# Kernel tuning notes

Hardware: AMD Instinct MI355X
Metric: run time of the kernel (lower is better)

## Reference

```python
import jax, jax.numpy as jnp
import numpy as np

NINP, NHID, K = 300, 64, 2   # input dim, hidden dim, pyramid levels (from Net.__init__)
GH = NHID // K               # per-pyramid-level width contributed to each gate (32)
S, B = 512, 256              # seq_len, batch


def setup_inputs() -> dict:
    key = jax.random.key(0)
    k = jax.random.split(key, 5)
    s = 0.05
    return {
        "x": jax.random.normal(k[0], (S, B, NINP), jnp.float32),
        "h0": jnp.zeros((B, NHID), jnp.float32),
        "c0": jnp.zeros((B, NHID), jnp.float32),
        "W_pt0": jax.random.normal(k[1], (NINP, 4 * GH), jnp.float32) * s,
        "b_pt0": jnp.zeros((4 * GH,), jnp.float32),
        "W_pt1": jax.random.normal(k[2], (NINP // 2, 4 * GH), jnp.float32) * s,
        "b_pt1": jnp.zeros((4 * GH,), jnp.float32),
        "W_glt": jax.random.normal(k[3], (1, NHID, 4 * NHID), jnp.float32) * s,  # g=1 grouped linear
        "W_dec": jax.random.normal(k[4], (NHID, 3), jnp.float32) * s,
        "b_dec": jnp.zeros((3,), jnp.float32),
    }


def _pyramidal_i2h(x, W_pt0, b_pt0, W_pt1, b_pt1):
    # Pyramidal transform: level 0 = full-res input, level 1 = features avg-pooled by 2.
    # Each level produces 4*GH gate features; levels are concatenated per gate -> NHID.
    x1 = x.reshape(x.shape[0], x.shape[1], NINP // 2, 2).mean(-1)  # (S,B,150)
    g0 = (x @ W_pt0 + b_pt0).reshape(x.shape[0], x.shape[1], 4, GH)
    g1 = (x1 @ W_pt1 + b_pt1).reshape(x.shape[0], x.shape[1], 4, GH)
    return jnp.concatenate([g0, g1], axis=-1)  # (S,B,4,NHID) gates order: f,g,i,o


def reference(x, h0, c0, W_pt0, b_pt0, W_pt1, b_pt1, W_glt, W_dec, b_dec):
    # Precompute input-to-hidden gate contributions for all timesteps (same math as per-step).
    i2h = _pyramidal_i2h(x, W_pt0, b_pt0, W_pt1, b_pt1)  # (S,B,4,NHID)
    bsz = h0.shape[0]

    def step(carry, i2h_t):
        h, c = carry
        # grouped linear (g=1): (B,1,NHID) x (1,NHID,4*NHID) -> (B,4,NHID)
        h2h = jnp.einsum('bgi,gio->bgo', h.reshape(bsz, 1, NHID), W_glt).reshape(bsz, 4, NHID)
        gates = i2h_t + h2h
        f, g, i, o = gates[:, 0], gates[:, 1], gates[:, 2], gates[:, 3]
        c1 = jax.nn.sigmoid(f) * c + jax.nn.sigmoid(i) * jnp.tanh(g)
        h1 = jax.nn.sigmoid(o) * jnp.tanh(c1)
        return (h1, c1), h1

    (hT, cT), hs = jax.lax.scan(step, (h0, c0), i2h)  # hs: (S,B,NHID)
    decoded = hs @ W_dec + b_dec                       # (S,B,3)
    return decoded, hT, cT
```

## Files before the change

### kernel.cpp

```cpp
#include <hip/hip_runtime.h>
#include <hip/hip_bf16.h>

#define SLEN 512
#define BATCH 256
#define NIN 300
#define KP 320
#define NG 256
#define NH 64
#define BM 128
#define BN 128
#define BK 64
#define LDP 72

typedef float f32x4 __attribute__((ext_vector_type(4)));
typedef _Float16 f16x8 __attribute__((ext_vector_type(8)));
typedef _Float16 f16x4 __attribute__((ext_vector_type(4)));

__global__ void prep_w(const float* __restrict__ Wpt0, const float* __restrict__ bpt0,
                       const float* __restrict__ Wpt1, const float* __restrict__ bpt1,
                       const float* __restrict__ Wglt,
                       _Float16* __restrict__ Wc16, float* __restrict__ bcat,
                       _Float16* __restrict__ Wg16) {
  int idx = blockIdx.x * 256 + threadIdx.x;
  if (idx < NG * KP) {
    int n = idx / KP, k = idx - n * KP;
    int g = n >> 6, h = n & 63;
    float w = 0.f;
    if (k < NIN) {
      if (h < 32) w = Wpt0[k * 128 + g * 32 + h];
      else        w = 0.5f * Wpt1[(k >> 1) * 128 + g * 32 + (h - 32)];
    }
    Wc16[idx] = (_Float16)w;
  }
  if (idx < NG * NH) {
    int c = idx >> 6, k = idx & 63;
    Wg16[idx] = (_Float16)Wglt[k * NG + c];
  }
  if (idx < NG) {
    int g = idx >> 6, h = idx & 63;
    bcat[idx] = (h < 32) ? bpt0[g * 32 + h] : bpt1[g * 32 + h - 32];
  }
}

__global__ __launch_bounds__(256) void gemm_i2h(
    const float* __restrict__ x, const _Float16* __restrict__ Wc16,
    const float* __restrict__ bcat, _Float16* __restrict__ C) {
  __shared__ _Float16 As[BM][LDP];
  __shared__ _Float16 Bs[BN][LDP];
  const int tid = threadIdx.x;
  const int m0 = blockIdx.y * BM;
  const int n0 = blockIdx.x * BN;
  const int lane = tid & 63;
  const int w = tid >> 6;
  const int wr = w >> 1, wc = w & 1;

  f32x4 acc[4][4];
#pragma unroll
  for (int m = 0; m < 4; ++m)
#pragma unroll
    for (int n = 0; n < 4; ++n) acc[m][n] = (f32x4){0.f, 0.f, 0.f, 0.f};

  const int arow_l = tid >> 4;
  const int acol   = (tid & 15) * 4;
  const int brow_l = tid >> 3;
  const int bcol   = (tid & 7) * 8;

  for (int k0 = 0; k0 < KP; k0 += BK) {
#pragma unroll
    for (int p = 0; p < 8; ++p) {
      int row = p * 16 + arow_l;
      int gk = k0 + acol;
      f32x4 v = (f32x4){0.f, 0.f, 0.f, 0.f};
      if (gk + 3 < NIN)
        v = *reinterpret_cast<const f32x4*>(&x[(size_t)(m0 + row) * NIN + gk]);
      f16x4 sv;
      sv[0] = (_Float16)v[0]; sv[1] = (_Float16)v[1];
      sv[2] = (_Float16)v[2]; sv[3] = (_Float16)v[3];
      *reinterpret_cast<f16x4*>(&As[row][acol]) = sv;
    }
#pragma unroll
    for (int p = 0; p < 4; ++p) {
      int n = p * 32 + brow_l;
      f16x8 v = *reinterpret_cast<const f16x8*>(&Wc16[(size_t)(n0 + n) * KP + k0 + bcol]);
      *reinterpret_cast<f16x8*>(&Bs[n][bcol]) = v;
    }
    __syncthreads();
#pragma unroll
    for (int ks = 0; ks < 2; ++ks) {
      const int kk = ks * 32 + (lane >> 4) * 8;
      f16x8 a[4], b[4];
#pragma unroll
      for (int m = 0; m < 4; ++m)
        a[m] = *reinterpret_cast<const f16x8*>(&As[wr * 64 + m * 16 + (lane & 15)][kk]);
#pragma unroll
      for (int n = 0; n < 4; ++n)
        b[n] = *reinterpret_cast<const f16x8*>(&Bs[wc * 64 + n * 16 + (lane & 15)][kk]);
#pragma unroll
      for (int m = 0; m < 4; ++m)
#pragma unroll
        for (int n = 0; n < 4; ++n)
          acc[m][n] = __builtin_amdgcn_mfma_f32_16x16x32_f16(a[m], b[n], acc[m][n], 0, 0, 0);
    }
    __syncthreads();
  }
  const int fc = lane & 15;
  const int fr = (lane >> 4) * 4;
#pragma unroll
  for (int n = 0; n < 4; ++n) {
    int col = n0 + wc * 64 + n * 16 + fc;
    float bias = bcat[col];
#pragma unroll
    for (int m = 0; m < 4; ++m) {
#pragma unroll
      for (int r = 0; r < 4; ++r) {
        int row = m0 + wr * 64 + m * 16 + fr + r;
        C[(size_t)row * NG + col] = (_Float16)(acc[m][n][r] + bias);
      }
    }
  }
}

__global__ __launch_bounds__(256, 4)
void rec_seq(
    const _Float16* __restrict__ i2h, const _Float16* __restrict__ Wg16,
    const float* __restrict__ h_in, const float* __restrict__ c_in,
    float* __restrict__ h_state, float* __restrict__ c_state,
    _Float16* __restrict__ hs_out, float* __restrict__ hT_out, float* __restrict__ cT_out,
    int T, int is_last) {
  const int b = blockIdx.x;
  const int tid = threadIdx.x;
  const int ww = tid >> 6;
  const int l = tid & 63;
  const int g = l >> 4;
  const int hidx = ww * 16 + (l & 15);
  const int col = g * 64 + hidx;

  __shared__ __align__(16) char LB[8 * NG * 16];
  f16x8* Wst = reinterpret_cast<f16x8*>(LB);
  _Float16* hbuf = reinterpret_cast<_Float16*>(LB);

  for (int e = tid; e < 8 * NG; e += 256) {
    int kk = e >> 8, c = e & 255;
    Wst[e] = *reinterpret_cast<const f16x8*>(Wg16 + (size_t)c * NH + kk * 8);
  }
  __syncthreads();

  f16x8 w0 = Wst[0 * NG + col], w1 = Wst[1 * NG + col];
  f16x8 w2 = Wst[2 * NG + col], w3 = Wst[3 * NG + col];
  f16x8 w4 = Wst[4 * NG + col], w5 = Wst[5 * NG + col];
  f16x8 w6 = Wst[6 * NG + col], w7 = Wst[7 * NG + col];

  float creg = 0.f, hreg = 0.f;
  if (l < 16) creg = c_in[b * NH + hidx];
  float h0v = (tid < NH) ? h_in[b * NH + tid] : 0.f;
  __syncthreads();

  if (tid < NH) hbuf[tid] = (_Float16)h0v;
  __syncthreads();

  const size_t st = (size_t)NG * BATCH;
  const unsigned short* ip =
      reinterpret_cast<const unsigned short*>(i2h) + (size_t)b * NG + col;
  _Float16* hp = hs_out + (size_t)b * NH + hidx;
  const float mm = (g == 1) ? 2.f : 1.f;

#define PAIR(v, j) __builtin_shufflevector(v, v, 2*(j), 2*(j)+1)
#define DOT(hb, i, W) { f16x8 hv = (hb)[i]; \
      acc0 = __builtin_amdgcn_fdot2(PAIR(hv,0), PAIR(W,0), acc0, false); \
      acc1 = __builtin_amdgcn_fdot2(PAIR(hv,1), PAIR(W,1), acc1, false); \
      acc0 = __builtin_amdgcn_fdot2(PAIR(hv,2), PAIR(W,2), acc0, false); \
      acc1 = __builtin_amdgcn_fdot2(PAIR(hv,3), PAIR(W,3), acc1, false); }

#define STEP(CUR, SP) { \
    float cur_ = (float)__builtin_bit_cast(_Float16, (unsigned short)(CUR)); \
    const f16x8* hb = reinterpret_cast<const f16x8*>(hbuf + ((SP) & 1) * NH); \
    float acc0 = 0.f, acc1 = 0.f; \
    DOT(hb, 0, w0) DOT(hb, 1, w1) DOT(hb, 2, w2) DOT(hb, 3, w3) \
    DOT(hb, 4, w4) DOT(hb, 5, w5) DOT(hb, 6, w6) DOT(hb, 7, w7) \
    float pre = cur_ + (acc0 + acc1); \
    float xx = fminf(fmaxf(pre, -30.f), 30.f); \
    float e = __expf(-mm * xx); \
    float y = 1.f / (1.f + e); \
    float act = (g == 1) ? (2.f * y - 1.f) : y; \
    float g_ = __shfl(act, l + 16); \
    float i_ = __shfl(act, l + 32); \
    float o_ = __shfl(act, l + 48); \
    if (l < 16) { \
      float c1 = act * creg + i_ * g_; \
      creg = c1; \
      float ct = fminf(fmaxf(c1, -15.f), 15.f); \
      float e2 = __expf(-2.f * ct); \
      float th = (1.f - e2) / (1.f + e2); \
      float h1 = o_ * th; \
      hreg = h1; \
      hbuf[(((SP) + 1) & 1) * NH + hidx] = (_Float16)h1; \
      *hp = (_Float16)h1;   \
    } \
    hp += st >> 2;  \
    asm volatile("s_waitcnt lgkmcnt(0)" ::: "memory"); \
    __builtin_amdgcn_s_barrier(); }

  int s = 0;
  if (T >= 8) {
    unsigned short c0v = ip[0],      c1v = ip[st],     c2v = ip[2 * st], c3v = ip[3 * st];
    unsigned short n0v = ip[4 * st], n1v = ip[5 * st], n2v = ip[6 * st], n3v = ip[7 * st];
    const unsigned short* ipf = ip + 8 * st;
    while (s + 4 <= T) {
      unsigned short f0v = 0, f1v = 0, f2v = 0, f3v = 0;
      if (s + 8  < T) f0v = ipf[0];
      if (s + 9  < T) f1v = ipf[st];
      if (s + 10 < T) f2v = ipf[2 * st];
      if (s + 11 < T) f3v = ipf[3 * st];
      ipf += 4 * st;
      STEP(c0v, s)
      STEP(c1v, s + 1)
      STEP(c2v, s + 2)
      STEP(c3v, s + 3)
      c0v = n0v; c1v = n1v; c2v = n2v; c3v = n3v;
      n0v = f0v; n1v = f1v; n2v = f2v; n3v = f3v;
      s += 4;
    }
    if (s < T) { STEP(c0v, s) s++; }
    if (s < T) { STEP(c1v, s) s++; }
    if (s < T) { STEP(c2v, s) s++; }
  } else {
    while (s < T) { unsigned short cv = ip[(size_t)s * st]; STEP(cv, s) s++; }
  }

  if (l < 16) {
    h_state[b * NH + hidx] = hreg;
    c_state[b * NH + hidx] = creg;
    if (is_last) {
      hT_out[b * NH + hidx] = hreg;
      cT_out[b * NH + hidx] = creg;
    }
  }
}

__global__ __launch_bounds__(256) void decode(
    const _Float16* __restrict__ hs, const float* __restrict__ Wdec,
    const float* __restrict__ bdec, float* __restrict__ out) {
  __shared__ float wl[NH * 3];
  __shared__ float bl[3];
  __shared__ float ob[256 * 3];
  const int tid = threadIdx.x;
  if (tid < NH * 3) wl[tid] = Wdec[tid];
  if (tid < 3) bl[tid] = bdec[tid];
  __syncthreads();
  const size_t idx = (size_t)blockIdx.x * 256 + tid;
  const _Float16* hp = hs + idx * NH;
  float d0 = 0.f, d1 = 0.f, d2 = 0.f;
#pragma unroll
  for (int k = 0; k < NH; k += 8) {
    f16x8 h8 = *reinterpret_cast<const f16x8*>(&hp[k]);
#pragma unroll
    for (int j = 0; j < 8; ++j) {
      float hv = (float)h8[j];
      d0 += hv * wl[(k + j) * 3 + 0];
      d1 += hv * wl[(k + j) * 3 + 1];
      d2 += hv * wl[(k + j) * 3 + 2];
    }
  }
  ob[tid * 3 + 0] = d0 + bl[0];
  ob[tid * 3 + 1] = d1 + bl[1];
  ob[tid * 3 + 2] = d2 + bl[2];
  __syncthreads();
  if (tid < 192) {
    f32x4* o4 = reinterpret_cast<f32x4*>(out + (size_t)blockIdx.x * 768);
    o4[tid] = reinterpret_cast<const f32x4*>(ob)[tid];
  }
}

extern "C" void kernel_launch(void* const* d_in, const int* in_sizes, int n_in,
                              void* d_out, int out_size, void* d_ws, size_t ws_size,
                              hipStream_t stream) {
  const float* x    = (const float*)d_in[0];
  const float* h0   = (const float*)d_in[1];
  const float* c0   = (const float*)d_in[2];
  const float* Wpt0 = (const float*)d_in[3];
  const float* bpt0 = (const float*)d_in[4];
  const float* Wpt1 = (const float*)d_in[5];
  const float* bpt1 = (const float*)d_in[6];
  const float* Wglt = (const float*)d_in[7];
  const float* Wdec = (const float*)d_in[8];
  const float* bdec = (const float*)d_in[9];
  float* out = (float*)d_out;

  char* ws = (char*)d_ws;
  _Float16*  Wc16    = (_Float16*)(ws);
  float*     bcat    = (float*)(ws + 163840);
  _Float16*  Wg16    = (_Float16*)(ws + 164864);
  float*     h_state = (float*)(ws + 197632);
  float*     c_state = (float*)(ws + 263168);
  const size_t base = 328704;

  const size_t i2h_step = (size_t)BATCH * NG * 2;
  const size_t hs_step  = (size_t)BATCH * NH * 2;
  size_t avail = (ws_size > base) ? ws_size - base : 0;
  int T = (int)(avail / (i2h_step + hs_step));
  if (T > SLEN) T = SLEN;
  if (T < 1) T = 1;

  _Float16* i2h = (_Float16*)(ws + base);
  _Float16* hs  = (_Float16*)(ws + base + (size_t)T * i2h_step);

  prep_w<<<dim3((NG * KP + 255) / 256), dim3(256), 0, stream>>>(
      Wpt0, bpt0, Wpt1, bpt1, Wglt, Wc16, bcat, Wg16);

  for (int t0 = 0; t0 < SLEN; t0 += T) {
    int Tc = (SLEN - t0 < T) ? (SLEN - t0) : T;
    dim3 g(NG / BN, Tc * BATCH / BM);
    gemm_i2h<<<g, dim3(256), 0, stream>>>(
        x + (size_t)t0 * BATCH * NIN, Wc16, bcat, i2h);
    rec_seq<<<dim3(BATCH), dim3(256), 0, stream>>>(
        i2h, Wg16,
        (t0 == 0) ? h0 : h_state, (t0 == 0) ? c0 : c_state,
        h_state, c_state, hs,
        out + (size_t)SLEN * BATCH * 3,
        out + (size_t)SLEN * BATCH * 3 + BATCH * NH,
        Tc, (t0 + Tc >= SLEN) ? 1 : 0);
    decode<<<dim3(Tc * BATCH / 256), dim3(256), 0, stream>>>(
        hs, Wdec, bdec, out + (size_t)t0 * BATCH * 3);
  }
}
```

Before: 293.0 us.

## Fuse recurrence, next-chunk GEMM and previous-chunk decode into one pipelined kernel

Measured after the change: 276.9 us. -5.5%, faster.

```diff
diff --git a/kernel.cpp b/kernel.cpp
--- a/kernel.cpp
+++ b/kernel.cpp
@@ -11,6 +11,8 @@
 #define BN 128
 #define BK 64
 #define LDP 72
+#define TC 128
+#define NCH (SLEN / TC)
 
 typedef float f32x4 __attribute__((ext_vector_type(4)));
 typedef _Float16 f16x8 __attribute__((ext_vector_type(8)));
@@ -42,14 +44,13 @@
   }
 }
 
-__global__ __launch_bounds__(256) void gemm_i2h(
+
+__device__ __forceinline__ void gemm_body(
+    char* LB, int m0, int n0, int tid,
     const float* __restrict__ x, const _Float16* __restrict__ Wc16,
     const float* __restrict__ bcat, _Float16* __restrict__ C) {
-  __shared__ _Float16 As[BM][LDP];
-  __shared__ _Float16 Bs[BN][LDP];
-  const int tid = threadIdx.x;
-  const int m0 = blockIdx.y * BM;
-  const int n0 = blockIdx.x * BN;
+  _Float16 (*As)[LDP] = reinterpret_cast<_Float16(*)[LDP]>(LB);
+  _Float16 (*Bs)[LDP] = reinterpret_cast<_Float16(*)[LDP]>(LB + BM * LDP * 2);
   const int lane = tid & 63;
   const int w = tid >> 6;
   const int wr = w >> 1, wc = w & 1;
@@ -120,49 +121,39 @@
   }
 }
 
-__global__ __launch_bounds__(256, 4)
-void rec_seq(
-    const _Float16* __restrict__ i2h, const _Float16* __restrict__ Wg16,
-    const float* __restrict__ h_in, const float* __restrict__ c_in,
-    float* __restrict__ h_state, float* __restrict__ c_state,
-    _Float16* __restrict__ hs_out, float* __restrict__ hT_out, float* __restrict__ cT_out,
-    int T, int is_last) {
-  const int b = blockIdx.x;
-  const int tid = threadIdx.x;
-  const int ww = tid >> 6;
-  const int l = tid & 63;
-  const int g = l >> 4;
-  const int hidx = ww * 16 + (l & 15);
-  const int col = g * 64 + hidx;
-
-  __shared__ __align__(16) char LB[8 * NG * 16];
-  f16x8* Wst = reinterpret_cast<f16x8*>(LB);
-  _Float16* hbuf = reinterpret_cast<_Float16*>(LB);
-
-  for (int e = tid; e < 8 * NG; e += 256) {
-    int kk = e >> 8, c = e & 255;
-    Wst[e] = *reinterpret_cast<const f16x8*>(Wg16 + (size_t)c * NH + kk * 8);
-  }
+__device__ __forceinline__ void decode_body(
+    char* LB, int blk, int tid,
+    const _Float16* __restrict__ hs, const float* __restrict__ Wdec,
+    const float* __restrict__ bdec, float* __restrict__ out) {
+  float* wl = reinterpret_cast<float*>(LB);
+  float* bl = reinterpret_cast<float*>(LB + 768);
+  float* ob = reinterpret_cast<float*>(LB + 784);
+  if (tid < NH * 3) wl[tid] = Wdec[tid];
+  if (tid < 3) bl[tid] = bdec[tid];
   __syncthreads();
-
-  f16x8 w0 = Wst[0 * NG + col], w1 = Wst[1 * NG + col];
-  f16x8 w2 = Wst[2 * NG + col], w3 = Wst[3 * NG + col];
-  f16x8 w4 = Wst[4 * NG + col], w5 = Wst[5 * NG + col];
-  f16x8 w6 = Wst[6 * NG + col], w7 = Wst[7 * NG + col];
-
-  float creg = 0.f, hreg = 0.f;
-  if (l < 16) creg = c_in[b * NH + hidx];
-  float h0v = (tid < NH) ? h_in[b * NH + tid] : 0.f;
+  const size_t idx = (size_t)blk * 256 + tid;
+  const _Float16* hp = hs + idx * NH;
+  float d0 = 0.f, d1 = 0.f, d2 = 0.f;
+#pragma unroll
+  for (int k = 0; k < NH; k += 8) {
+    f16x8 h8 = *reinterpret_cast<const f16x8*>(&hp[k]);
+#pragma unroll
+    for (int j = 0; j < 8; ++j) {
+      float hv = (float)h8[j];
+      d0 += hv * wl[(k + j) * 3 + 0];
+      d1 += hv * wl[(k + j) * 3 + 1];
+      d2 += hv * wl[(k + j) * 3 + 2];
+    }
+  }
+  ob[tid * 3 + 0] = d0 + bl[0];
+  ob[tid * 3 + 1] = d1 + bl[1];
+  ob[tid * 3 + 2] = d2 + bl[2];
   __syncthreads();
-
-  if (tid < NH) hbuf[tid] = (_Float16)h0v;
-  __syncthreads();
-
-  const size_t st = (size_t)NG * BATCH;
-  const unsigned short* ip =
-      reinterpret_cast<const unsigned short*>(i2h) + (size_t)b * NG + col;
-  _Float16* hp = hs_out + (size_t)b * NH + hidx;
-  const float mm = (g == 1) ? 2.f : 1.f;
+  if (tid < 192) {
+    f32x4* o4 = reinterpret_cast<f32x4*>(out + (size_t)blk * 768);
+    o4[tid] = reinterpret_cast<const f32x4*>(ob)[tid];
+  }
+}
 
 #define PAIR(v, j) __builtin_shufflevector(v, v, 2*(j), 2*(j)+1)
 #define DOT(hb, i, W) { f16x8 hv = (hb)[i]; \
@@ -200,74 +191,112 @@
     asm volatile("s_waitcnt lgkmcnt(0)" ::: "memory"); \
     __builtin_amdgcn_s_barrier(); }
 
-  int s = 0;
-  if (T >= 8) {
-    unsigned short c0v = ip[0],      c1v = ip[st],     c2v = ip[2 * st], c3v = ip[3 * st];
-    unsigned short n0v = ip[4 * st], n1v = ip[5 * st], n2v = ip[6 * st], n3v = ip[7 * st];
-    const unsigned short* ipf = ip + 8 * st;
-    while (s + 4 <= T) {
-      unsigned short f0v = 0, f1v = 0, f2v = 0, f3v = 0;
-      if (s + 8  < T) f0v = ipf[0];
-      if (s + 9  < T) f1v = ipf[st];
-      if (s + 10 < T) f2v = ipf[2 * st];
-      if (s + 11 < T) f3v = ipf[3 * st];
-      ipf += 4 * st;
-      STEP(c0v, s)
-      STEP(c1v, s + 1)
-      STEP(c2v, s + 2)
-      STEP(c3v, s + 3)
-      c0v = n0v; c1v = n1v; c2v = n2v; c3v = n3v;
-      n0v = f0v; n1v = f1v; n2v = f2v; n3v = f3v;
-      s += 4;
-    }
-    if (s < T) { STEP(c0v, s) s++; }
-    if (s < T) { STEP(c1v, s) s++; }
-    if (s < T) { STEP(c2v, s) s++; }
-  } else {
-    while (s < T) { unsigned short cv = ip[(size_t)s * st]; STEP(cv, s) s++; }
-  }
-
-  if (l < 16) {
-    h_state[b * NH + hidx] = hreg;
-    c_state[b * NH + hidx] = creg;
-    if (is_last) {
-      hT_out[b * NH + hidx] = hreg;
-      cT_out[b * NH + hidx] = creg;
-    }
-  }
+
+__global__ __launch_bounds__(256, 2) void gemm_i2h(
+    const float* __restrict__ x, const _Float16* __restrict__ Wc16,
+    const float* __restrict__ bcat, _Float16* __restrict__ C) {
+  __shared__ __align__(16) char LB[36864];
+  gemm_body(LB, blockIdx.y * BM, blockIdx.x * BN, threadIdx.x, x, Wc16, bcat, C);
 }
 
 __global__ __launch_bounds__(256) void decode(
     const _Float16* __restrict__ hs, const float* __restrict__ Wdec,
     const float* __restrict__ bdec, float* __restrict__ out) {
-  __shared__ float wl[NH * 3];
-  __shared__ float bl[3];
-  __shared__ float ob[256 * 3];
+  __shared__ __align__(16) char LB[4096];
+  decode_body(LB, blockIdx.x, threadIdx.x, hs, Wdec, bdec, out);
+}
+
+__global__ __launch_bounds__(256, 2)
+void fused_step(
+    const _Float16* __restrict__ i2h_cur, _Float16* __restrict__ i2h_next,
+    const float* __restrict__ x_next,
+    const _Float16* __restrict__ Wc16, const float* __restrict__ bcat,
+    const _Float16* __restrict__ Wg16,
+    const float* __restrict__ h_in, const float* __restrict__ c_in,
+    float* __restrict__ h_state, float* __restrict__ c_state,
+    _Float16* __restrict__ hs_cur, const _Float16* __restrict__ hs_prev,
+    const float* __restrict__ Wdec, const float* __restrict__ bdec,
+    float* __restrict__ out_prev,
+    float* __restrict__ hT_out, float* __restrict__ cT_out,
+    int is_last, int has_gemm) {
+  __shared__ __align__(16) char LB[36864];
+  const int bid = blockIdx.x;
   const int tid = threadIdx.x;
-  if (tid < NH * 3) wl[tid] = Wdec[tid];
-  if (tid < 3) bl[tid] = bdec[tid];
-  __syncthreads();
-  const size_t idx = (size_t)blockIdx.x * 256 + tid;
-  const _Float16* hp = hs + idx * NH;
-  float d0 = 0.f, d1 = 0.f, d2 = 0.f;
-#pragma unroll
-  for (int k = 0; k < NH; k += 8) {
-    f16x8 h8 = *reinterpret_cast<const f16x8*>(&hp[k]);
-#pragma unroll
-    for (int j = 0; j < 8; ++j) {
-      float hv = (float)h8[j];
-      d0 += hv * wl[(k + j) * 3 + 0];
-      d1 += hv * wl[(k + j) * 3 + 1];
-      d2 += hv * wl[(k + j) * 3 + 2];
-    }
-  }
-  ob[tid * 3 + 0] = d0 + bl[0];
-  ob[tid * 3 + 1] = d1 + bl[1];
-  ob[tid * 3 + 2] = d2 + bl[2];
-  __syncthreads();
-  if (tid < 192) {
-    f32x4* o4 = reinterpret_cast<f32x4*>(out + (size_t)blockIdx.x * 768);
-    o4[tid] = reinterpret_cast<const f32x4*>(ob)[tid];
+
+  if (bid < BATCH) {
+    const int b = bid;
+    const int ww = tid >> 6;
+    const int l = tid & 63;
+    const int g = l >> 4;
+    const int hidx = ww * 16 + (l & 15);
+    const int col = g * 64 + hidx;
+
+    f16x8* Wst = reinterpret_cast<f16x8*>(LB);
+    _Float16* hbuf = reinterpret_cast<_Float16*>(LB);
+
+    for (int e = tid; e < 8 * NG; e += 256) {
+      int kk = e >> 8, c = e & 255;
+      Wst[e] = *reinterpret_cast<const f16x8*>(Wg16 + (size_t)c * NH + kk * 8);
+    }
+    __syncthreads();
+
+    f16x8 w0 = Wst[0 * NG + col], w1 = Wst[1 * NG + col];
+    f16x8 w2 = Wst[2 * NG + col], w3 = Wst[3 * NG + col];
+    f16x8 w4 = Wst[4 * NG + col], w5 = Wst[5 * NG + col];
+    f16x8 w6 = Wst[6 * NG + col], w7 = Wst[7 * NG + col];
+
+    float creg = 0.f, hreg = 0.f;
+    if (l < 16) creg = c_in[b * NH + hidx];
+    float h0v = (tid < NH) ? h_in[b * NH + tid] : 0.f;
+    __syncthreads();
+
+    if (tid < NH) hbuf[tid] = (_Float16)h0v;
+    __syncthreads();
+
+    const size_t st = (size_t)NG * BATCH;
+    const unsigned short* ip =
+        reinterpret_cast<const unsigned short*>(i2h_cur) + (size_t)b * NG + col;
+    _Float16* hp = hs_cur + (size_t)b * NH + hidx;
+    const float mm = (g == 1) ? 2.f : 1.f;
+
+    int s = 0;
+    {
+      unsigned short c0v = ip[0],      c1v = ip[st],     c2v = ip[2 * st], c3v = ip[3 * st];
+      unsigned short n0v = ip[4 * st], n1v = ip[5 * st], n2v = ip[6 * st], n3v = ip[7 * st];
+      const unsigned short* ipf = ip + 8 * st;
+      while (s + 4 <= TC) {
+        unsigned short f0v = 0, f1v = 0, f2v = 0, f3v = 0;
+        if (s + 8  < TC) f0v = ipf[0];
+        if (s + 9  < TC) f1v = ipf[st];
+        if (s + 10 < TC) f2v = ipf[2 * st];
+        if (s + 11 < TC) f3v = ipf[3 * st];
+        ipf += 4 * st;
+        STEP(c0v, s)
+        STEP(c1v, s + 1)
+        STEP(c2v, s + 2)
+        STEP(c3v, s + 3)
+        c0v = n0v; c1v = n1v; c2v = n2v; c3v = n3v;
+        n0v = f0v; n1v = f1v; n2v = f2v; n3v = f3v;
+        s += 4;
+      }
+    }
+
+    if (l < 16) {
+      h_state[b * NH + hidx] = hreg;
+      c_state[b * NH + hidx] = creg;
+      if (is_last) {
+        hT_out[b * NH + hidx] = hreg;
+        cT_out[b * NH + hidx] = creg;
+      }
+    }
+  } else if (has_gemm && bid < BATCH + 2 * (TC * BATCH / BM)) {
+    const int gid = bid - BATCH;
+    const int n0 = (gid & 1) * BN;
+    const int m0 = (gid >> 1) * BM;
+    gemm_body(LB, m0, n0, tid, x_next, Wc16, bcat, i2h_next);
+  } else {
+    const int did = bid - BATCH - (has_gemm ? 2 * (TC * BATCH / BM) : 0);
+    decode_body(LB, did, tid, hs_prev, Wdec, bdec, out_prev);
   }
 }
 
@@ -294,32 +323,40 @@
   float*     c_state = (float*)(ws + 263168);
   const size_t base = 328704;
 
-  const size_t i2h_step = (size_t)BATCH * NG * 2;
-  const size_t hs_step  = (size_t)BATCH * NH * 2;
-  size_t avail = (ws_size > base) ? ws_size - base : 0;
-  int T = (int)(avail / (i2h_step + hs_step));
-  if (T > SLEN) T = SLEN;
-  if (T < 1) T = 1;
-
-  _Float16* i2h = (_Float16*)(ws + base);
-  _Float16* hs  = (_Float16*)(ws + base + (size_t)T * i2h_step);
+  const size_t chunk_i2h = (size_t)TC * BATCH * NG;
+  _Float16* i2h0 = (_Float16*)(ws + base);
+  _Float16* i2h1 = i2h0 + chunk_i2h;
+  _Float16* hs   = (_Float16*)(ws + base + 4 * chunk_i2h);
 
   prep_w<<<dim3((NG * KP + 255) / 256), dim3(256), 0, stream>>>(
       Wpt0, bpt0, Wpt1, bpt1, Wglt, Wc16, bcat, Wg16);
 
-  for (int t0 = 0; t0 < SLEN; t0 += T) {
-    int Tc = (SLEN - t0 < T) ? (SLEN - t0) : T;
-    dim3 g(NG / BN, Tc * BATCH / BM);
-    gemm_i2h<<<g, dim3(256), 0, stream>>>(
-        x + (size_t)t0 * BATCH * NIN, Wc16, bcat, i2h);
-    rec_seq<<<dim3(BATCH), dim3(256), 0, stream>>>(
-        i2h, Wg16,
-        (t0 == 0) ? h0 : h_state, (t0 == 0) ? c0 : c_state,
-        h_state, c_state, hs,
+  gemm_i2h<<<dim3(2, TC * BATCH / BM), dim3(256), 0, stream>>>(
+      x, Wc16, bcat, i2h0);
+
+  for (int k = 0; k < NCH; ++k) {
+    _Float16* cur = (k & 1) ? i2h1 : i2h0;
+    _Float16* nxt = (k & 1) ? i2h0 : i2h1;
+    const int has_gemm = (k + 1 < NCH) ? 1 : 0;
+    const int has_dec  = (k > 0) ? 1 : 0;
+    const int nblk = BATCH + (has_gemm ? 2 * (TC * BATCH / BM) : 0)
+                           + (has_dec ? (TC * BATCH / 256) : 0);
+    const int kp = (k > 0) ? (k - 1) : 0;
+    fused_step<<<dim3(nblk), dim3(256), 0, stream>>>(
+        cur, nxt, x + (size_t)(k + 1) * TC * BATCH * NIN,
+        Wc16, bcat, Wg16,
+        (k == 0) ? h0 : h_state, (k == 0) ? c0 : c_state,
+        h_state, c_state,
+        hs + (size_t)k * TC * BATCH * NH,
+        hs + (size_t)kp * TC * BATCH * NH,
+        Wdec, bdec,
+        out + (size_t)kp * TC * BATCH * 3,
         out + (size_t)SLEN * BATCH * 3,
         out + (size_t)SLEN * BATCH * 3 + BATCH * NH,
-        Tc, (t0 + Tc >= SLEN) ? 1 : 0);
-    decode<<<dim3(Tc * BATCH / 256), dim3(256), 0, stream>>>(
-        hs, Wdec, bdec, out + (size_t)t0 * BATCH * 3);
-  }
-}
+        (k == NCH - 1) ? 1 : 0, has_gemm);
+  }
+
+  decode<<<dim3(TC * BATCH / 256), dim3(256), 0, stream>>>(
+      hs + (size_t)(NCH - 1) * TC * BATCH * NH, Wdec, bdec,
+      out + (size_t)(NCH - 1) * TC * BATCH * 3);
+}
```
